# Performance work log

Measured on AMD Instinct MI355X. Metric: run time of the kernel, lower is better.

The kernel has to match this reference:

```python
import jax, jax.numpy as jnp
import numpy as np

N_USER = 200000
N_ITEM = 100000
N_NODES = N_USER + N_ITEM
EMB = 80            # embed_size; divisible by 5
FEAT = EMB // 5     # 16, per-feature embedding dim
N_LAYER = 3
NNZ = 1_000_000
BATCH = 4096
EMB_RATIO = 0.5
NEG_SLOPE = 0.2
EPS = 1e-12         # F.normalize clamp_min eps


def setup_inputs() -> dict:
    key = jax.random.key(0)
    ks = jax.random.split(key, 24)
    inp = {}
    inp["u_id"] = jax.random.randint(ks[0], (BATCH,), 0, N_USER)
    inp["age"] = jax.random.randint(ks[1], (BATCH,), 0, 10)
    inp["sex"] = jax.random.randint(ks[2], (BATCH,), 0, 2)
    inp["month"] = jax.random.randint(ks[3], (BATCH,), 0, 12)
    inp["day"] = jax.random.randint(ks[4], (BATCH,), 0, 31)
    inp["dow"] = jax.random.randint(ks[5], (BATCH,), 0, 7)
    inp["pos_item"] = jax.random.randint(ks[6], (BATCH,), 0, N_ITEM)
    inp["neg_item"] = jax.random.randint(ks[7], (BATCH,), 0, N_ITEM)
    # COO sparse Laplacian (one entry of lap_list)
    inp["lap_rows"] = jax.random.randint(ks[8], (NNZ,), 0, N_NODES)
    inp["lap_cols"] = jax.random.randint(ks[9], (NNZ,), 0, N_NODES)
    inp["lap_vals"] = jax.random.uniform(ks[10], (NNZ,), jnp.float32) * 0.01
    # learned parameters (kaiming-uniform-ish scale)
    inp["user_tab"] = jax.random.normal(ks[11], (N_USER, EMB), jnp.float32) * 0.1
    inp["item_tab"] = jax.random.normal(ks[12], (N_ITEM, EMB), jnp.float32) * 0.1
    inp["age_tab"] = jax.random.normal(ks[13], (10, FEAT), jnp.float32) * 0.1
    inp["sex_tab"] = jax.random.normal(ks[14], (2, FEAT), jnp.float32) * 0.1
    inp["month_tab"] = jax.random.normal(ks[15], (12, FEAT), jnp.float32) * 0.1
    inp["day_tab"] = jax.random.normal(ks[16], (31, FEAT), jnp.float32) * 0.1
    inp["dow_tab"] = jax.random.normal(ks[17], (7, FEAT), jnp.float32) * 0.1
    s = 1.0 / np.sqrt(EMB)
    inp["W1"] = jax.random.uniform(ks[18], (N_LAYER, EMB, EMB), jnp.float32, -s, s)
    inp["b1"] = jax.random.uniform(ks[19], (N_LAYER, EMB), jnp.float32, -s, s)
    inp["W2"] = jax.random.uniform(ks[20], (N_LAYER, EMB, EMB), jnp.float32, -s, s)
    inp["b2"] = jax.random.uniform(ks[21], (N_LAYER, EMB), jnp.float32, -s, s)
    return inp


def reference(u_id, age, sex, month, day, dow, pos_item, neg_item,
              lap_rows, lap_cols, lap_vals,
              user_tab, item_tab, age_tab, sex_tab, month_tab, day_tab, dow_tab,
              W1, b1, W2, b2):
    # demographic/date feature vector, concat order matches torch forward
    feats = jnp.concatenate(
        [age_tab[age], sex_tab[sex], month_tab[month], day_tab[day], dow_tab[dow]],
        axis=1)  # [B, EMB]
    # in-place .data blend of user rows (feats are detached in torch)
    blend = user_tab[u_id] * (1.0 - EMB_RATIO) + jax.lax.stop_gradient(feats) * EMB_RATIO
    updated = user_tab.at[u_id].set(blend)
    # torch mutates .data: values change, autograd sees identity -> same trick here
    user_eff = user_tab + jax.lax.stop_gradient(updated - user_tab)

    E = jnp.concatenate([user_eff, item_tab], axis=0)  # [N, EMB]
    all_E = [E]
    for i in range(N_LAYER):  # eval mode: node/message dropout off (node_flag=False)
        # sparse Laplacian matmul: L_E[r] = sum_nnz vals * E[cols]
        L_E = jax.ops.segment_sum(lap_vals[:, None] * E[lap_cols], lap_rows,
                                  num_segments=N_NODES)
        # L_E@W1+b1 + E@W1+b1 + (L_E*E)@W2+b2  (bias b1 intentionally twice, as in source)
        msg = (L_E + E) @ W1[i] + 2.0 * b1[i] + (L_E * E) @ W2[i] + b2[i]
        E = jax.nn.leaky_relu(msg, NEG_SLOPE)
        norm = E / jnp.maximum(jnp.linalg.norm(E, axis=1, keepdims=True), EPS)
        all_E.append(norm)
    all_E = jnp.concatenate(all_E, axis=1)  # [N, EMB*(L+1)]

    users = all_E[:N_USER]
    items = all_E[N_USER:]
    return users[u_id], items[pos_item], items[neg_item]
```

## Files before the change

kernel.cpp:

```cpp
#include <hip/hip_runtime.h>
#include <hip/hip_bf16.h>

#define N_USER 200000
#define N_ITEM 100000
#define N_NODES 300000
#define EMB 80
#define FEAT 16
#define NL 3
#define NNZ 1000000
#define BATCH 4096
#define OUTW 320

typedef __bf16 bf16x8 __attribute__((ext_vector_type(8)));
typedef float f32x4 __attribute__((ext_vector_type(4)));

__device__ __forceinline__ unsigned short f2bf(float f){
  union { float f; unsigned int i; } x; x.f = f;
  unsigned int i = x.i;
  unsigned int r = i + 0x7fff + ((i >> 16) & 1u);
  return (unsigned short)(r >> 16);
}
__device__ __forceinline__ float bf2f_lo(unsigned int u){
  union { unsigned int i; float f; } x; x.i = u << 16; return x.f;
}
__device__ __forceinline__ float bf2f_hi(unsigned int u){
  union { unsigned int i; float f; } x; x.i = u & 0xffff0000u; return x.f;
}

__device__ __forceinline__ void acc8(f32x4* a, uint4 u, float v){
  a[0].x += v*bf2f_lo(u.x); a[0].y += v*bf2f_hi(u.x);
  a[0].z += v*bf2f_lo(u.y); a[0].w += v*bf2f_hi(u.y);
  a[1].x += v*bf2f_lo(u.z); a[1].y += v*bf2f_hi(u.z);
  a[1].z += v*bf2f_lo(u.w); a[1].w += v*bf2f_hi(u.w);
}

__device__ __forceinline__ void combine_store(unsigned short* lp_add, unsigned short* lp_mul,
                                              const f32x4* a, uint4 u){
  float e0=bf2f_lo(u.x), e1=bf2f_hi(u.x), e2=bf2f_lo(u.y), e3=bf2f_hi(u.y);
  float e4=bf2f_lo(u.z), e5=bf2f_hi(u.z), e6=bf2f_lo(u.w), e7=bf2f_hi(u.w);
  bf16x8 av, mv;
  av[0]=(__bf16)(a[0].x+e0); av[1]=(__bf16)(a[0].y+e1);
  av[2]=(__bf16)(a[0].z+e2); av[3]=(__bf16)(a[0].w+e3);
  av[4]=(__bf16)(a[1].x+e4); av[5]=(__bf16)(a[1].y+e5);
  av[6]=(__bf16)(a[1].z+e6); av[7]=(__bf16)(a[1].w+e7);
  mv[0]=(__bf16)(a[0].x*e0); mv[1]=(__bf16)(a[0].y*e1);
  mv[2]=(__bf16)(a[0].z*e2); mv[3]=(__bf16)(a[0].w*e3);
  mv[4]=(__bf16)(a[1].x*e4); mv[5]=(__bf16)(a[1].y*e5);
  mv[6]=(__bf16)(a[1].z*e6); mv[7]=(__bf16)(a[1].w*e7);
  *(bf16x8*)lp_add = av;
  *(bf16x8*)lp_mul = mv;
}

__global__ void k_fill(float* out, int n, float v){
  int i = blockIdx.x * blockDim.x + threadIdx.x;
  if (i < n) out[i] = v;
}

__global__ void k_winner(const int* __restrict__ u_id, int* __restrict__ winner){
  int b = blockIdx.x * blockDim.x + threadIdx.x;
  if (b >= BATCH) return;
  atomicMax(&winner[u_id[b]], b);
}

__global__ void k_copy_bf(const float4* __restrict__ user_tab, const float4* __restrict__ item_tab,
                          uint2* __restrict__ EB){
  int idx = blockIdx.x * blockDim.x + threadIdx.x;
  if (idx >= N_NODES*EMB/4) return;
  float4 v = (idx < N_USER*EMB/4) ? user_tab[idx] : item_tab[idx - N_USER*EMB/4];
  uint2 o;
  o.x = (unsigned int)f2bf(v.x) | ((unsigned int)f2bf(v.y) << 16);
  o.y = (unsigned int)f2bf(v.z) | ((unsigned int)f2bf(v.w) << 16);
  EB[idx] = o;
}

__global__ void k_scatter_blend(const int* __restrict__ u_id, const int* __restrict__ winner,
                        const int* __restrict__ age, const int* __restrict__ sex,
                        const int* __restrict__ month, const int* __restrict__ day,
                        const int* __restrict__ dow,
                        const float* __restrict__ user_tab,
                        const float* __restrict__ age_tab, const float* __restrict__ sex_tab,
                        const float* __restrict__ month_tab, const float* __restrict__ day_tab,
                        const float* __restrict__ dow_tab,
                        unsigned short* __restrict__ EB){
  int idx = blockIdx.x * blockDim.x + threadIdx.x;
  if (idx >= BATCH*EMB) return;
  int b = idx / EMB;
  int c = idx - b*EMB;
  int u = u_id[b];
  if (winner[u] != b) return;
  int t = c >> 4, cc = c & 15;
  int key; const float* tab;
  switch (t){
    case 0: key = age[b];   tab = age_tab;   break;
    case 1: key = sex[b];   tab = sex_tab;   break;
    case 2: key = month[b]; tab = month_tab; break;
    case 3: key = day[b];   tab = day_tab;   break;
    default: key = dow[b];  tab = dow_tab;   break;
  }
  float f = tab[key*FEAT + cc];
  EB[(size_t)u*EMB + c] = f2bf(0.5f * user_tab[(size_t)u*EMB + c] + 0.5f * f);
}

__global__ void k_prep(const float* __restrict__ W1, const float* __restrict__ W2,
                       const float* __restrict__ b1, const float* __restrict__ b2,
                       unsigned short* __restrict__ Wt, float* __restrict__ biasf){
  int idx = blockIdx.x * blockDim.x + threadIdx.x;
  if (idx < NL*EMB*160){
    int i = idx / (EMB*160);
    int rem = idx - i*(EMB*160);
    int n = rem / 160;
    int k = rem - n*160;
    float v = (k < EMB) ? W1[i*EMB*EMB + k*EMB + n] : W2[i*EMB*EMB + (k-EMB)*EMB + n];
    Wt[idx] = f2bf(v);
  } else if (idx < NL*EMB*160 + NL*EMB){
    int t = idx - NL*EMB*160;
    biasf[t] = 2.0f * b1[t] + b2[t];
  }
}

__global__ void k_hist(const int* __restrict__ rows, int* __restrict__ cnt){
  int e = blockIdx.x * blockDim.x + threadIdx.x;
  if (e < NNZ) atomicAdd(&cnt[rows[e]], 1);
}

#define SCAN_BLK 1024
__global__ void k_scan1(int* __restrict__ cnt, int* __restrict__ bsum){
  __shared__ int s[256];
  int tid = threadIdx.x;
  int base = blockIdx.x * SCAN_BLK + tid*4;
  int v[4]; int sum = 0;
  #pragma unroll
  for (int j = 0; j < 4; j++){
    int i = base + j;
    v[j] = (i < N_NODES) ? cnt[i] : 0;
    sum += v[j];
  }
  s[tid] = sum; __syncthreads();
  int own = sum;
  for (int d = 1; d < 256; d <<= 1){
    int t = (tid >= d) ? s[tid-d] : 0;
    __syncthreads();
    s[tid] += t;
    __syncthreads();
  }
  int excl = s[tid] - own;
  if (tid == 0) bsum[blockIdx.x] = s[255];
  int run = excl;
  #pragma unroll
  for (int j = 0; j < 4; j++){
    int i = base + j;
    if (i < N_NODES) cnt[i] = run;
    run += v[j];
  }
}

#define NSCAN_BLOCKS ((N_NODES + SCAN_BLK - 1)/SCAN_BLK)
__global__ void k_scan2(int* __restrict__ bsum){
  __shared__ int s[512];
  int tid = threadIdx.x;
  int v = (tid < NSCAN_BLOCKS) ? bsum[tid] : 0;
  s[tid] = v; __syncthreads();
  for (int d = 1; d < 512; d <<= 1){
    int t = (tid >= d) ? s[tid-d] : 0;
    __syncthreads();
    s[tid] += t;
    __syncthreads();
  }
  if (tid < NSCAN_BLOCKS) bsum[tid] = s[tid] - v;
}

__global__ void k_scan3(int* __restrict__ rowptr, const int* __restrict__ bsum,
                        int* __restrict__ cursor){
  int i = blockIdx.x * blockDim.x + threadIdx.x;
  if (i >= N_NODES) return;
  int v = rowptr[i] + bsum[i >> 10];
  rowptr[i] = v;
  cursor[i] = v;
  if (i == 0) rowptr[N_NODES] = NNZ;
}

__global__ void k_scatter_edges(const int* __restrict__ rows, const int* __restrict__ cols,
                                const float* __restrict__ vals,
                                int* __restrict__ cursor,
                                int2* __restrict__ edges){
  int e = blockIdx.x * blockDim.x + threadIdx.x;
  if (e >= NNZ) return;
  int r = rows[e];
  int pos = atomicAdd(&cursor[r], 1);
  int2 ed; ed.x = cols[e]; ed.y = __float_as_int(vals[e]);
  edges[pos] = ed;
}

#define LE_STRIDE 168
__launch_bounds__(256)
__global__ void k_fused2(const unsigned short* __restrict__ EBin, unsigned short* __restrict__ EBout,
                         const int* __restrict__ rowptr, const int2* __restrict__ edges,
                         const unsigned short* __restrict__ Wt, const float* __restrict__ biasf){
  __shared__ unsigned short la[64 * LE_STRIDE];
  int tid = threadIdx.x;
  long row0 = (long)blockIdx.x * 64;

  int lane = tid & 63;
  int wave = tid >> 6;
  int m = lane & 15;
  int quad = lane >> 4;

  {
    int lr = tid >> 2;
    int qg = tid & 3;
    long r = row0 + lr;
    int s = 0, e = 0;
    if (r < N_NODES){ s = rowptr[r]; e = rowptr[r+1]; }
    int eo = 8*qg;
    f32x4 c0[2], c1[2], c2[2];
    c0[0]=(f32x4){0,0,0,0}; c0[1]=(f32x4){0,0,0,0};
    c1[0]=(f32x4){0,0,0,0}; c1[1]=(f32x4){0,0,0,0};
    c2[0]=(f32x4){0,0,0,0}; c2[1]=(f32x4){0,0,0,0};
    int ilast = e - 1;
    for (int i = s; i < e; i += 4){
      int rem = e - i;
      int2 ed0 = edges[i];
      int2 ed1 = edges[min(i+1, ilast)];
      int2 ed2 = edges[min(i+2, ilast)];
      int2 ed3 = edges[min(i+3, ilast)];
      float v0 = __int_as_float(ed0.y);
      float v1 = (rem > 1) ? __int_as_float(ed1.y) : 0.f;
      float v2 = (rem > 2) ? __int_as_float(ed2.y) : 0.f;
      float v3 = (rem > 3) ? __int_as_float(ed3.y) : 0.f;
      const unsigned short* g0 = EBin + (size_t)ed0.x*EMB + eo;
      const unsigned short* g1 = EBin + (size_t)ed1.x*EMB + eo;
      const unsigned short* g2 = EBin + (size_t)ed2.x*EMB + eo;
      const unsigned short* g3 = EBin + (size_t)ed3.x*EMB + eo;
      {
        uint4 u0 = *(const uint4*)(g0);
        uint4 u1 = *(const uint4*)(g1);
        uint4 u2 = *(const uint4*)(g2);
        uint4 u3 = *(const uint4*)(g3);
        acc8(c0, u0, v0); acc8(c0, u1, v1); acc8(c0, u2, v2); acc8(c0, u3, v3);
      }
      {
        uint4 u0 = *(const uint4*)(g0 + 32);
        uint4 u1 = *(const uint4*)(g1 + 32);
        uint4 u2 = *(const uint4*)(g2 + 32);
        uint4 u3 = *(const uint4*)(g3 + 32);
        acc8(c1, u0, v0); acc8(c1, u1, v1); acc8(c1, u2, v2); acc8(c1, u3, v3);
      }
      if (qg < 2){
        uint4 u0 = *(const uint4*)(g0 + 64);
        uint4 u1 = *(const uint4*)(g1 + 64);
        uint4 u2 = *(const uint4*)(g2 + 64);
        uint4 u3 = *(const uint4*)(g3 + 64);
        acc8(c2, u0, v0); acc8(c2, u1, v1); acc8(c2, u2, v2); acc8(c2, u3, v3);
      }
    }
    const unsigned short* myrow = EBin + (size_t)(r < N_NODES ? r : 0) * EMB;
    unsigned short* lp = la + lr*LE_STRIDE;
    {
      uint4 u = *(const uint4*)(myrow + eo);
      combine_store(lp + eo, lp + 80 + eo, c0, u);
    }
    {
      uint4 u = *(const uint4*)(myrow + 32 + eo);
      combine_store(lp + 32 + eo, lp + 80 + 32 + eo, c1, u);
    }
    if (qg < 2){
      uint4 u = *(const uint4*)(myrow + 64 + eo);
      combine_store(lp + 64 + eo, lp + 80 + 64 + eo, c2, u);
    }
  }

  bf16x8 bfrag[5][5];
  #pragma unroll
  for (int nt = 0; nt < 5; nt++)
    #pragma unroll
    for (int kt = 0; kt < 5; kt++)
      bfrag[nt][kt] = *(const bf16x8*)(Wt + (nt*16 + m)*160 + kt*32 + quad*8);

  asm volatile("s_waitcnt lgkmcnt(0)" ::: "memory");
  __builtin_amdgcn_sched_barrier(0);

  int arow = wave*16 + m;
  const unsigned short* lA = la + arow*LE_STRIDE;

  f32x4 acc[5];
  #pragma unroll
  for (int nt = 0; nt < 5; nt++) acc[nt] = (f32x4){0.f,0.f,0.f,0.f};

  #pragma unroll
  for (int kt = 0; kt < 5; kt++){
    bf16x8 af = *(const bf16x8*)(lA + kt*32 + quad*8);
    #pragma unroll
    for (int nt = 0; nt < 5; nt++)
      acc[nt] = __builtin_amdgcn_mfma_f32_16x16x32_bf16(af, bfrag[nt][kt], acc[nt], 0, 0, 0);
  }

  long rbase = row0 + wave*16 + quad*4;
  #pragma unroll
  for (int nt = 0; nt < 5; nt++){
    int col = nt*16 + m;
    float b = biasf[col];
    #pragma unroll
    for (int i = 0; i < 4; i++){
      long r = rbase + i;
      if (r < N_NODES){
        float v = acc[nt][i] + b;
        v = (v > 0.f) ? v : 0.2f * v;
        EBout[r*EMB + col] = f2bf(v);
      }
    }
  }
}

__global__ void k_gather_wave(const unsigned short* __restrict__ EB, const int* __restrict__ u_id,
                              const int* __restrict__ pos, const int* __restrict__ neg,
                              float* __restrict__ out, int layer, int do_norm){
  int gw = blockIdx.x * (blockDim.x >> 6) + (threadIdx.x >> 6);
  if (gw >= 3*BATCH) return;
  int lane = threadIdx.x & 63;
  int chunk = gw / BATCH;
  int b = gw - chunk*BATCH;
  int node = (chunk == 0) ? u_id[b] : ((chunk == 1) ? N_USER + pos[b] : N_USER + neg[b]);
  const unsigned short* er = EB + (size_t)node*EMB;
  union { unsigned int i; float f; } c0, c1;
  c0.i = (unsigned int)er[lane] << 16;
  float v0 = c0.f;
  float v1 = 0.f;
  if (lane < EMB-64){ c1.i = (unsigned int)er[64 + lane] << 16; v1 = c1.f; }
  float scale = 1.f;
  if (do_norm){
    float ss = v0*v0 + v1*v1;
    #pragma unroll
    for (int s = 32; s > 0; s >>= 1) ss += __shfl_xor(ss, s, 64);
    float nrm = fmaxf(sqrtf(ss), 1e-12f);
    scale = 1.f / nrm;
  }
  float* po = out + (size_t)chunk*BATCH*OUTW + (size_t)b*OUTW + layer*EMB;
  po[lane] = v0 * scale;
  if (lane < EMB-64) po[64 + lane] = v1 * scale;
}

extern "C" void kernel_launch(void* const* d_in, const int* in_sizes, int n_in,
                              void* d_out, int out_size, void* d_ws, size_t ws_size,
                              hipStream_t stream) {
  float* out = (float*)d_out;

  const size_t OFF_EB0    = 0;
  const size_t OFF_EB1    = 48000000;
  const size_t OFF_ROWPTR = 96000000;
  const size_t OFF_CURSOR = 97200640;
  const size_t OFF_EDGES  = 98401280;
  const size_t OFF_BSUM   = 106401280;
  const size_t OFF_WT     = 106405376;
  const size_t OFF_BIAS   = 106482176;
  const size_t OFF_WIN    = 106483200;
  const size_t NEED       = 107283200;

  float code = 0.f;
  if (ws_size < NEED)                      code = 7.f;
  else if (n_in != 22)                     code = 9.f;
  else if (in_sizes[0] != BATCH)           code = 11.f;
  else if (in_sizes[10] != NNZ)            code = 13.f;
  else if (out_size != 3*BATCH*OUTW)       code = 19.f;
  if (code != 0.f){
    k_fill<<<(out_size + 255)/256, 256, 0, stream>>>(out, out_size, code);
    return;
  }

  const int* u_id  = (const int*)d_in[0];
  const int* age   = (const int*)d_in[1];
  const int* sex   = (const int*)d_in[2];
  const int* month = (const int*)d_in[3];
  const int* day   = (const int*)d_in[4];
  const int* dow   = (const int*)d_in[5];
  const int* pos   = (const int*)d_in[6];
  const int* neg   = (const int*)d_in[7];
  const int* lrows = (const int*)d_in[8];
  const int* lcols = (const int*)d_in[9];
  const float* lvals    = (const float*)d_in[10];
  const float* user_tab = (const float*)d_in[11];
  const float* item_tab = (const float*)d_in[12];
  const float* age_tab  = (const float*)d_in[13];
  const float* sex_tab  = (const float*)d_in[14];
  const float* month_tab= (const float*)d_in[15];
  const float* day_tab  = (const float*)d_in[16];
  const float* dow_tab  = (const float*)d_in[17];
  const float* W1 = (const float*)d_in[18];
  const float* b1 = (const float*)d_in[19];
  const float* W2 = (const float*)d_in[20];
  const float* b2 = (const float*)d_in[21];

  char* ws = (char*)d_ws;
  unsigned short* EB0 = (unsigned short*)(ws + OFF_EB0);
  unsigned short* EB1 = (unsigned short*)(ws + OFF_EB1);
  int* rowptr   = (int*)(ws + OFF_ROWPTR);
  int* cursor   = (int*)(ws + OFF_CURSOR);
  int2* edges   = (int2*)(ws + OFF_EDGES);
  int* bsum     = (int*)(ws + OFF_BSUM);
  unsigned short* Wt = (unsigned short*)(ws + OFF_WT);
  float* biasf  = (float*)(ws + OFF_BIAS);
  int* winner   = (int*)(ws + OFF_WIN);

  hipMemsetAsync(winner, 0xFF, N_USER*sizeof(int), stream);
  k_winner<<<(BATCH+255)/256, 256, 0, stream>>>(u_id, winner);
  k_copy_bf<<<(N_NODES*EMB/4+255)/256, 256, 0, stream>>>((const float4*)user_tab, (const float4*)item_tab, (uint2*)EB0);
  k_scatter_blend<<<(BATCH*EMB+255)/256, 256, 0, stream>>>(u_id, winner, age, sex, month, day, dow,
                                                   user_tab, age_tab, sex_tab, month_tab,
                                                   day_tab, dow_tab, EB0);
  k_prep<<<(NL*EMB*160 + NL*EMB + 255)/256, 256, 0, stream>>>(W1, W2, b1, b2, Wt, biasf);

  hipMemsetAsync(rowptr, 0, (N_NODES+1)*sizeof(int), stream);
  k_hist<<<(NNZ+255)/256, 256, 0, stream>>>(lrows, rowptr);
  k_scan1<<<NSCAN_BLOCKS, 256, 0, stream>>>(rowptr, bsum);
  k_scan2<<<1, 512, 0, stream>>>(bsum);
  k_scan3<<<(N_NODES+255)/256, 256, 0, stream>>>(rowptr, bsum, cursor);
  k_scatter_edges<<<(NNZ+255)/256, 256, 0, stream>>>(lrows, lcols, lvals, cursor, edges);

  k_gather_wave<<<(3*BATCH+3)/4, 256, 0, stream>>>(EB0, u_id, pos, neg, out, 0, 0);

  unsigned short* Ein = EB0; unsigned short* Eout = EB1;
  for (int i = 0; i < NL; i++){
    k_fused2<<<(N_NODES+63)/64, 256, 0, stream>>>(Ein, Eout, rowptr, edges,
                                                  Wt + i*EMB*160, biasf + i*EMB);
    k_gather_wave<<<(3*BATCH+3)/4, 256, 0, stream>>>(Eout, u_id, pos, neg, out, i+1, 1);
    unsigned short* t = Ein; Ein = Eout; Eout = t;
  }
}
```

Baseline: 580.0 us.

## Merge setup kernels into fewer launches and unroll edge gather to eight

Several setup kernels are merged into fewer launches. Two memsets become one init kernel, winner selection joins the row histogram, and the bf16 table copy, feature blend and weight prep become one build kernel. Edge scattering shares a launch with the layer-0 output gather. The SpMM edge loop now issues eight row gathers per iteration instead of four, for more memory-level parallelism. This trades launch and dependency overhead for more registers in the fused layer kernel and extra branching in the combined kernels.

```diff
diff --git a/kernel.cpp b/kernel.cpp
--- a/kernel.cpp
+++ b/kernel.cpp
@@ -56,71 +56,74 @@
   if (i < n) out[i] = v;
 }
 
-__global__ void k_winner(const int* __restrict__ u_id, int* __restrict__ winner){
-  int b = blockIdx.x * blockDim.x + threadIdx.x;
-  if (b >= BATCH) return;
-  atomicMax(&winner[u_id[b]], b);
-}
-
-__global__ void k_copy_bf(const float4* __restrict__ user_tab, const float4* __restrict__ item_tab,
-                          uint2* __restrict__ EB){
-  int idx = blockIdx.x * blockDim.x + threadIdx.x;
-  if (idx >= N_NODES*EMB/4) return;
-  float4 v = (idx < N_USER*EMB/4) ? user_tab[idx] : item_tab[idx - N_USER*EMB/4];
-  uint2 o;
-  o.x = (unsigned int)f2bf(v.x) | ((unsigned int)f2bf(v.y) << 16);
-  o.y = (unsigned int)f2bf(v.z) | ((unsigned int)f2bf(v.w) << 16);
-  EB[idx] = o;
-}
-
-__global__ void k_scatter_blend(const int* __restrict__ u_id, const int* __restrict__ winner,
+__global__ void k_init(int* __restrict__ winner, int* __restrict__ rowptr){
+  int i = blockIdx.x * blockDim.x + threadIdx.x;
+  if (i <= N_NODES) rowptr[i] = 0;
+  if (i < N_USER)   winner[i] = -1;
+}
+
+__global__ void k_winner_hist(const int* __restrict__ u_id, int* __restrict__ winner,
+                              const int* __restrict__ rows, int* __restrict__ cnt){
+  int i = blockIdx.x * blockDim.x + threadIdx.x;
+  if (i < BATCH) atomicMax(&winner[u_id[i]], i);
+  int e = i - BATCH;
+  if (e >= 0 && e < NNZ) atomicAdd(&cnt[rows[e]], 1);
+}
+
+__global__ void k_build(const float4* __restrict__ user_tab4, const float4* __restrict__ item_tab4,
+                        const int* __restrict__ winner,
                         const int* __restrict__ age, const int* __restrict__ sex,
                         const int* __restrict__ month, const int* __restrict__ day,
                         const int* __restrict__ dow,
-                        const float* __restrict__ user_tab,
                         const float* __restrict__ age_tab, const float* __restrict__ sex_tab,
                         const float* __restrict__ month_tab, const float* __restrict__ day_tab,
                         const float* __restrict__ dow_tab,
-                        unsigned short* __restrict__ EB){
+                        uint2* __restrict__ EB,
+                        const float* __restrict__ W1, const float* __restrict__ W2,
+                        const float* __restrict__ b1, const float* __restrict__ b2,
+                        unsigned short* __restrict__ Wt, float* __restrict__ biasf){
   int idx = blockIdx.x * blockDim.x + threadIdx.x;
-  if (idx >= BATCH*EMB) return;
-  int b = idx / EMB;
-  int c = idx - b*EMB;
-  int u = u_id[b];
-  if (winner[u] != b) return;
-  int t = c >> 4, cc = c & 15;
-  int key; const float* tab;
-  switch (t){
-    case 0: key = age[b];   tab = age_tab;   break;
-    case 1: key = sex[b];   tab = sex_tab;   break;
-    case 2: key = month[b]; tab = month_tab; break;
-    case 3: key = day[b];   tab = day_tab;   break;
-    default: key = dow[b];  tab = dow_tab;   break;
-  }
-  float f = tab[key*FEAT + cc];
-  EB[(size_t)u*EMB + c] = f2bf(0.5f * user_tab[(size_t)u*EMB + c] + 0.5f * f);
-}
-
-__global__ void k_prep(const float* __restrict__ W1, const float* __restrict__ W2,
-                       const float* __restrict__ b1, const float* __restrict__ b2,
-                       unsigned short* __restrict__ Wt, float* __restrict__ biasf){
-  int idx = blockIdx.x * blockDim.x + threadIdx.x;
-  if (idx < NL*EMB*160){
-    int i = idx / (EMB*160);
-    int rem = idx - i*(EMB*160);
-    int n = rem / 160;
-    int k = rem - n*160;
-    float v = (k < EMB) ? W1[i*EMB*EMB + k*EMB + n] : W2[i*EMB*EMB + (k-EMB)*EMB + n];
-    Wt[idx] = f2bf(v);
-  } else if (idx < NL*EMB*160 + NL*EMB){
-    int t = idx - NL*EMB*160;
-    biasf[t] = 2.0f * b1[t] + b2[t];
-  }
-}
-
-__global__ void k_hist(const int* __restrict__ rows, int* __restrict__ cnt){
-  int e = blockIdx.x * blockDim.x + threadIdx.x;
-  if (e < NNZ) atomicAdd(&cnt[rows[e]], 1);
+  if (idx < N_NODES*EMB/4){
+    float4 v = (idx < N_USER*EMB/4) ? user_tab4[idx] : item_tab4[idx - N_USER*EMB/4];
+    if (idx < N_USER*EMB/4){
+      int u = idx / 20;
+      int b = winner[u];
+      if (b >= 0){
+        int c = (idx - u*20) * 4;
+        int t = c >> 4, cc = c & 15;
+        int key; const float* tab;
+        switch (t){
+          case 0: key = age[b];   tab = age_tab;   break;
+          case 1: key = sex[b];   tab = sex_tab;   break;
+          case 2: key = month[b]; tab = month_tab; break;
+          case 3: key = day[b];   tab = day_tab;   break;
+          default: key = dow[b];  tab = dow_tab;   break;
+        }
+        const float* tp = tab + key*FEAT + cc;
+        v.x = 0.5f*v.x + 0.5f*tp[0];
+        v.y = 0.5f*v.y + 0.5f*tp[1];
+        v.z = 0.5f*v.z + 0.5f*tp[2];
+        v.w = 0.5f*v.w + 0.5f*tp[3];
+      }
+    }
+    uint2 o;
+    o.x = (unsigned int)f2bf(v.x) | ((unsigned int)f2bf(v.y) << 16);
+    o.y = (unsigned int)f2bf(v.z) | ((unsigned int)f2bf(v.w) << 16);
+    EB[idx] = o;
+  } else {
+    int p = idx - N_NODES*EMB/4;
+    if (p < NL*EMB*160){
+      int i = p / (EMB*160);
+      int rem = p - i*(EMB*160);
+      int n = rem / 160;
+      int k = rem - n*160;
+      float v = (k < EMB) ? W1[i*EMB*EMB + k*EMB + n] : W2[i*EMB*EMB + (k-EMB)*EMB + n];
+      Wt[p] = f2bf(v);
+    } else if (p < NL*EMB*160 + NL*EMB){
+      int t = p - NL*EMB*160;
+      biasf[t] = 2.0f * b1[t] + b2[t];
+    }
+  }
 }
 
 #define SCAN_BLK 1024
@@ -179,144 +182,11 @@
   if (i == 0) rowptr[N_NODES] = NNZ;
 }
 
-__global__ void k_scatter_edges(const int* __restrict__ rows, const int* __restrict__ cols,
-                                const float* __restrict__ vals,
-                                int* __restrict__ cursor,
-                                int2* __restrict__ edges){
-  int e = blockIdx.x * blockDim.x + threadIdx.x;
-  if (e >= NNZ) return;
-  int r = rows[e];
-  int pos = atomicAdd(&cursor[r], 1);
-  int2 ed; ed.x = cols[e]; ed.y = __float_as_int(vals[e]);
-  edges[pos] = ed;
-}
-
-#define LE_STRIDE 168
-__launch_bounds__(256)
-__global__ void k_fused2(const unsigned short* __restrict__ EBin, unsigned short* __restrict__ EBout,
-                         const int* __restrict__ rowptr, const int2* __restrict__ edges,
-                         const unsigned short* __restrict__ Wt, const float* __restrict__ biasf){
-  __shared__ unsigned short la[64 * LE_STRIDE];
-  int tid = threadIdx.x;
-  long row0 = (long)blockIdx.x * 64;
-
-  int lane = tid & 63;
-  int wave = tid >> 6;
-  int m = lane & 15;
-  int quad = lane >> 4;
-
-  {
-    int lr = tid >> 2;
-    int qg = tid & 3;
-    long r = row0 + lr;
-    int s = 0, e = 0;
-    if (r < N_NODES){ s = rowptr[r]; e = rowptr[r+1]; }
-    int eo = 8*qg;
-    f32x4 c0[2], c1[2], c2[2];
-    c0[0]=(f32x4){0,0,0,0}; c0[1]=(f32x4){0,0,0,0};
-    c1[0]=(f32x4){0,0,0,0}; c1[1]=(f32x4){0,0,0,0};
-    c2[0]=(f32x4){0,0,0,0}; c2[1]=(f32x4){0,0,0,0};
-    int ilast = e - 1;
-    for (int i = s; i < e; i += 4){
-      int rem = e - i;
-      int2 ed0 = edges[i];
-      int2 ed1 = edges[min(i+1, ilast)];
-      int2 ed2 = edges[min(i+2, ilast)];
-      int2 ed3 = edges[min(i+3, ilast)];
-      float v0 = __int_as_float(ed0.y);
-      float v1 = (rem > 1) ? __int_as_float(ed1.y) : 0.f;
-      float v2 = (rem > 2) ? __int_as_float(ed2.y) : 0.f;
-      float v3 = (rem > 3) ? __int_as_float(ed3.y) : 0.f;
-      const unsigned short* g0 = EBin + (size_t)ed0.x*EMB + eo;
-      const unsigned short* g1 = EBin + (size_t)ed1.x*EMB + eo;
-      const unsigned short* g2 = EBin + (size_t)ed2.x*EMB + eo;
-      const unsigned short* g3 = EBin + (size_t)ed3.x*EMB + eo;
-      {
-        uint4 u0 = *(const uint4*)(g0);
-        uint4 u1 = *(const uint4*)(g1);
-        uint4 u2 = *(const uint4*)(g2);
-        uint4 u3 = *(const uint4*)(g3);
-        acc8(c0, u0, v0); acc8(c0, u1, v1); acc8(c0, u2, v2); acc8(c0, u3, v3);
-      }
-      {
-        uint4 u0 = *(const uint4*)(g0 + 32);
-        uint4 u1 = *(const uint4*)(g1 + 32);
-        uint4 u2 = *(const uint4*)(g2 + 32);
-        uint4 u3 = *(const uint4*)(g3 + 32);
-        acc8(c1, u0, v0); acc8(c1, u1, v1); acc8(c1, u2, v2); acc8(c1, u3, v3);
-      }
-      if (qg < 2){
-        uint4 u0 = *(const uint4*)(g0 + 64);
-        uint4 u1 = *(const uint4*)(g1 + 64);
-        uint4 u2 = *(const uint4*)(g2 + 64);
-        uint4 u3 = *(const uint4*)(g3 + 64);
-        acc8(c2, u0, v0); acc8(c2, u1, v1); acc8(c2, u2, v2); acc8(c2, u3, v3);
-      }
-    }
-    const unsigned short* myrow = EBin + (size_t)(r < N_NODES ? r : 0) * EMB;
-    unsigned short* lp = la + lr*LE_STRIDE;
-    {
-      uint4 u = *(const uint4*)(myrow + eo);
-      combine_store(lp + eo, lp + 80 + eo, c0, u);
-    }
-    {
-      uint4 u = *(const uint4*)(myrow + 32 + eo);
-      combine_store(lp + 32 + eo, lp + 80 + 32 + eo, c1, u);
-    }
-    if (qg < 2){
-      uint4 u = *(const uint4*)(myrow + 64 + eo);
-      combine_store(lp + 64 + eo, lp + 80 + 64 + eo, c2, u);
-    }
-  }
-
-  bf16x8 bfrag[5][5];
-  #pragma unroll
-  for (int nt = 0; nt < 5; nt++)
-    #pragma unroll
-    for (int kt = 0; kt < 5; kt++)
-      bfrag[nt][kt] = *(const bf16x8*)(Wt + (nt*16 + m)*160 + kt*32 + quad*8);
-
-  asm volatile("s_waitcnt lgkmcnt(0)" ::: "memory");
-  __builtin_amdgcn_sched_barrier(0);
-
-  int arow = wave*16 + m;
-  const unsigned short* lA = la + arow*LE_STRIDE;
-
-  f32x4 acc[5];
-  #pragma unroll
-  for (int nt = 0; nt < 5; nt++) acc[nt] = (f32x4){0.f,0.f,0.f,0.f};
-
-  #pragma unroll
-  for (int kt = 0; kt < 5; kt++){
-    bf16x8 af = *(const bf16x8*)(lA + kt*32 + quad*8);
-    #pragma unroll
-    for (int nt = 0; nt < 5; nt++)
-      acc[nt] = __builtin_amdgcn_mfma_f32_16x16x32_bf16(af, bfrag[nt][kt], acc[nt], 0, 0, 0);
-  }
-
-  long rbase = row0 + wave*16 + quad*4;
-  #pragma unroll
-  for (int nt = 0; nt < 5; nt++){
-    int col = nt*16 + m;
-    float b = biasf[col];
-    #pragma unroll
-    for (int i = 0; i < 4; i++){
-      long r = rbase + i;
-      if (r < N_NODES){
-        float v = acc[nt][i] + b;
-        v = (v > 0.f) ? v : 0.2f * v;
-        EBout[r*EMB + col] = f2bf(v);
-      }
-    }
-  }
-}
-
-__global__ void k_gather_wave(const unsigned short* __restrict__ EB, const int* __restrict__ u_id,
-                              const int* __restrict__ pos, const int* __restrict__ neg,
-                              float* __restrict__ out, int layer, int do_norm){
-  int gw = blockIdx.x * (blockDim.x >> 6) + (threadIdx.x >> 6);
-  if (gw >= 3*BATCH) return;
-  int lane = threadIdx.x & 63;
+__device__ __forceinline__ void gather_one(const unsigned short* __restrict__ EB,
+                                           const int* __restrict__ u_id,
+                                           const int* __restrict__ pos, const int* __restrict__ neg,
+                                           float* __restrict__ out, int layer, int do_norm,
+                                           int gw, int lane){
   int chunk = gw / BATCH;
   int b = gw - chunk*BATCH;
   int node = (chunk == 0) ? u_id[b] : ((chunk == 1) ? N_USER + pos[b] : N_USER + neg[b]);
@@ -337,6 +207,183 @@
   float* po = out + (size_t)chunk*BATCH*OUTW + (size_t)b*OUTW + layer*EMB;
   po[lane] = v0 * scale;
   if (lane < EMB-64) po[64 + lane] = v1 * scale;
+}
+
+#define SC_BLOCKS ((NNZ + 255)/256)
+#define G0_BLOCKS ((3*BATCH)/4)
+__global__ void k_scatter_gather0(const int* __restrict__ rows, const int* __restrict__ cols,
+                                  const float* __restrict__ vals, int* __restrict__ cursor,
+                                  int2* __restrict__ edges,
+                                  const unsigned short* __restrict__ EB,
+                                  const int* __restrict__ u_id, const int* __restrict__ pos,
+                                  const int* __restrict__ neg, float* __restrict__ out){
+  if (blockIdx.x < SC_BLOCKS){
+    int e = blockIdx.x * 256 + threadIdx.x;
+    if (e >= NNZ) return;
+    int r = rows[e];
+    int p = atomicAdd(&cursor[r], 1);
+    int2 ed; ed.x = cols[e]; ed.y = __float_as_int(vals[e]);
+    edges[p] = ed;
+  } else {
+    int gb = blockIdx.x - SC_BLOCKS;
+    int gw = gb*4 + (threadIdx.x >> 6);
+    gather_one(EB, u_id, pos, neg, out, 0, 0, gw, threadIdx.x & 63);
+  }
+}
+
+#define LE_STRIDE 168
+__launch_bounds__(256)
+__global__ void k_fused2(const unsigned short* __restrict__ EBin, unsigned short* __restrict__ EBout,
+                         const int* __restrict__ rowptr, const int2* __restrict__ edges,
+                         const unsigned short* __restrict__ Wt, const float* __restrict__ biasf){
+  __shared__ unsigned short la[64 * LE_STRIDE];
+  int tid = threadIdx.x;
+  long row0 = (long)blockIdx.x * 64;
+
+  int lane = tid & 63;
+  int wave = tid >> 6;
+  int m = lane & 15;
+  int quad = lane >> 4;
+
+  {
+    int lr = tid >> 2;
+    int qg = tid & 3;
+    long r = row0 + lr;
+    int s = 0, e = 0;
+    if (r < N_NODES){ s = rowptr[r]; e = rowptr[r+1]; }
+    int eo = 8*qg;
+    f32x4 c0[2], c1[2], c2[2];
+    c0[0]=(f32x4){0,0,0,0}; c0[1]=(f32x4){0,0,0,0};
+    c1[0]=(f32x4){0,0,0,0}; c1[1]=(f32x4){0,0,0,0};
+    c2[0]=(f32x4){0,0,0,0}; c2[1]=(f32x4){0,0,0,0};
+    int ilast = e - 1;
+    for (int i = s; i < e; i += 8){
+      int rem = e - i;
+      int2 ed0 = edges[i];
+      int2 ed1 = edges[min(i+1, ilast)];
+      int2 ed2 = edges[min(i+2, ilast)];
+      int2 ed3 = edges[min(i+3, ilast)];
+      int2 ed4 = edges[min(i+4, ilast)];
+      int2 ed5 = edges[min(i+5, ilast)];
+      int2 ed6 = edges[min(i+6, ilast)];
+      int2 ed7 = edges[min(i+7, ilast)];
+      float v0 = __int_as_float(ed0.y);
+      float v1 = (rem > 1) ? __int_as_float(ed1.y) : 0.f;
+      float v2 = (rem > 2) ? __int_as_float(ed2.y) : 0.f;
+      float v3 = (rem > 3) ? __int_as_float(ed3.y) : 0.f;
+      float v4 = (rem > 4) ? __int_as_float(ed4.y) : 0.f;
+      float v5 = (rem > 5) ? __int_as_float(ed5.y) : 0.f;
+      float v6 = (rem > 6) ? __int_as_float(ed6.y) : 0.f;
+      float v7 = (rem > 7) ? __int_as_float(ed7.y) : 0.f;
+      const unsigned short* g0 = EBin + (size_t)ed0.x*EMB + eo;
+      const unsigned short* g1 = EBin + (size_t)ed1.x*EMB + eo;
+      const unsigned short* g2 = EBin + (size_t)ed2.x*EMB + eo;
+      const unsigned short* g3 = EBin + (size_t)ed3.x*EMB + eo;
+      const unsigned short* g4 = EBin + (size_t)ed4.x*EMB + eo;
+      const unsigned short* g5 = EBin + (size_t)ed5.x*EMB + eo;
+      const unsigned short* g6 = EBin + (size_t)ed6.x*EMB + eo;
+      const unsigned short* g7 = EBin + (size_t)ed7.x*EMB + eo;
+      {
+        uint4 u0 = *(const uint4*)(g0);
+        uint4 u1 = *(const uint4*)(g1);
+        uint4 u2 = *(const uint4*)(g2);
+        uint4 u3 = *(const uint4*)(g3);
+        uint4 u4 = *(const uint4*)(g4);
+        uint4 u5 = *(const uint4*)(g5);
+        uint4 u6 = *(const uint4*)(g6);
+        uint4 u7 = *(const uint4*)(g7);
+        acc8(c0, u0, v0); acc8(c0, u1, v1); acc8(c0, u2, v2); acc8(c0, u3, v3);
+        acc8(c0, u4, v4); acc8(c0, u5, v5); acc8(c0, u6, v6); acc8(c0, u7, v7);
+      }
+      {
+        uint4 u0 = *(const uint4*)(g0 + 32);
+        uint4 u1 = *(const uint4*)(g1 + 32);
+        uint4 u2 = *(const uint4*)(g2 + 32);
+        uint4 u3 = *(const uint4*)(g3 + 32);
+        uint4 u4 = *(const uint4*)(g4 + 32);
+        uint4 u5 = *(const uint4*)(g5 + 32);
+        uint4 u6 = *(const uint4*)(g6 + 32);
+        uint4 u7 = *(const uint4*)(g7 + 32);
+        acc8(c1, u0, v0); acc8(c1, u1, v1); acc8(c1, u2, v2); acc8(c1, u3, v3);
+        acc8(c1, u4, v4); acc8(c1, u5, v5); acc8(c1, u6, v6); acc8(c1, u7, v7);
+      }
+      if (qg < 2){
+        uint4 u0 = *(const uint4*)(g0 + 64);
+        uint4 u1 = *(const uint4*)(g1 + 64);
+        uint4 u2 = *(const uint4*)(g2 + 64);
+        uint4 u3 = *(const uint4*)(g3 + 64);
+        uint4 u4 = *(const uint4*)(g4 + 64);
+        uint4 u5 = *(const uint4*)(g5 + 64);
+        uint4 u6 = *(const uint4*)(g6 + 64);
+        uint4 u7 = *(const uint4*)(g7 + 64);
+        acc8(c2, u0, v0); acc8(c2, u1, v1); acc8(c2, u2, v2); acc8(c2, u3, v3);
+        acc8(c2, u4, v4); acc8(c2, u5, v5); acc8(c2, u6, v6); acc8(c2, u7, v7);
+      }
+    }
+    const unsigned short* myrow = EBin + (size_t)(r < N_NODES ? r : 0) * EMB;
+    unsigned short* lp = la + lr*LE_STRIDE;
+    {
+      uint4 u = *(const uint4*)(myrow + eo);
+      combine_store(lp + eo, lp + 80 + eo, c0, u);
+    }
+    {
+      uint4 u = *(const uint4*)(myrow + 32 + eo);
+      combine_store(lp + 32 + eo, lp + 80 + 32 + eo, c1, u);
+    }
+    if (qg < 2){
+      uint4 u = *(const uint4*)(myrow + 64 + eo);
+      combine_store(lp + 64 + eo, lp + 80 + 64 + eo, c2, u);
+    }
+  }
+
+  bf16x8 bfrag[5][5];
+  #pragma unroll
+  for (int nt = 0; nt < 5; nt++)
+    #pragma unroll
+    for (int kt = 0; kt < 5; kt++)
+      bfrag[nt][kt] = *(const bf16x8*)(Wt + (nt*16 + m)*160 + kt*32 + quad*8);
+
+  asm volatile("s_waitcnt lgkmcnt(0)" ::: "memory");
+  __builtin_amdgcn_sched_barrier(0);
+
+  int arow = wave*16 + m;
+  const unsigned short* lA = la + arow*LE_STRIDE;
+
+  f32x4 acc[5];
+  #pragma unroll
+  for (int nt = 0; nt < 5; nt++) acc[nt] = (f32x4){0.f,0.f,0.f,0.f};
+
+  #pragma unroll
+  for (int kt = 0; kt < 5; kt++){
+    bf16x8 af = *(const bf16x8*)(lA + kt*32 + quad*8);
+    #pragma unroll
+    for (int nt = 0; nt < 5; nt++)
+      acc[nt] = __builtin_amdgcn_mfma_f32_16x16x32_bf16(af, bfrag[nt][kt], acc[nt], 0, 0, 0);
+  }
+
+  long rbase = row0 + wave*16 + quad*4;
+  #pragma unroll
+  for (int nt = 0; nt < 5; nt++){
+    int col = nt*16 + m;
+    float b = biasf[col];
+    #pragma unroll
+    for (int i = 0; i < 4; i++){
+      long r = rbase + i;
+      if (r < N_NODES){
+        float v = acc[nt][i] + b;
+        v = (v > 0.f) ? v : 0.2f * v;
+        EBout[r*EMB + col] = f2bf(v);
+      }
+    }
+  }
+}
+
+__global__ void k_gather_wave(const unsigned short* __restrict__ EB, const int* __restrict__ u_id,
+                              const int* __restrict__ pos, const int* __restrict__ neg,
+                              float* __restrict__ out, int layer, int do_norm){
+  int gw = blockIdx.x * (blockDim.x >> 6) + (threadIdx.x >> 6);
+  if (gw >= 3*BATCH) return;
+  gather_one(EB, u_id, pos, neg, out, layer, do_norm, gw, threadIdx.x & 63);
 }
 
 extern "C" void kernel_launch(void* const* d_in, const int* in_sizes, int n_in,
@@ -400,22 +447,17 @@
   float* biasf  = (float*)(ws + OFF_BIAS);
   int* winner   = (int*)(ws + OFF_WIN);
 
-  hipMemsetAsync(winner, 0xFF, N_USER*sizeof(int), stream);
-  k_winner<<<(BATCH+255)/256, 256, 0, stream>>>(u_id, winner);
-  k_copy_bf<<<(N_NODES*EMB/4+255)/256, 256, 0, stream>>>((const float4*)user_tab, (const float4*)item_tab, (uint2*)EB0);
-  k_scatter_blend<<<(BATCH*EMB+255)/256, 256, 0, stream>>>(u_id, winner, age, sex, month, day, dow,
-                                                   user_tab, age_tab, sex_tab, month_tab,
-                                                   day_tab, dow_tab, EB0);
-  k_prep<<<(NL*EMB*160 + NL*EMB + 255)/256, 256, 0, stream>>>(W1, W2, b1, b2, Wt, biasf);
-
-  hipMemsetAsync(rowptr, 0, (N_NODES+1)*sizeof(int), stream);
-  k_hist<<<(NNZ+255)/256, 256, 0, stream>>>(lrows, rowptr);
+  k_init<<<(N_NODES+1+255)/256, 256, 0, stream>>>(winner, rowptr);
+  k_winner_hist<<<(BATCH+NNZ+255)/256, 256, 0, stream>>>(u_id, winner, lrows, rowptr);
+  k_build<<<(N_NODES*EMB/4 + NL*EMB*160 + NL*EMB + 255)/256, 256, 0, stream>>>(
+      (const float4*)user_tab, (const float4*)item_tab, winner,
+      age, sex, month, day, dow, age_tab, sex_tab, month_tab, day_tab, dow_tab,
+      (uint2*)EB0, W1, W2, b1, b2, Wt, biasf);
   k_scan1<<<NSCAN_BLOCKS, 256, 0, stream>>>(rowptr, bsum);
   k_scan2<<<1, 512, 0, stream>>>(bsum);
   k_scan3<<<(N_NODES+255)/256, 256, 0, stream>>>(rowptr, bsum, cursor);
-  k_scatter_edges<<<(NNZ+255)/256, 256, 0, stream>>>(lrows, lcols, lvals, cursor, edges);
-
-  k_gather_wave<<<(3*BATCH+3)/4, 256, 0, stream>>>(EB0, u_id, pos, neg, out, 0, 0);
+  k_scatter_gather0<<<SC_BLOCKS + G0_BLOCKS, 256, 0, stream>>>(lrows, lcols, lvals, cursor,
+      edges, EB0, u_id, pos, neg, out);
 
   unsigned short* Ein = EB0; unsigned short* Eout = EB1;
   for (int i = 0; i < NL; i++){
```

After: 615.3 us. +6.1%, slower.
